# Performance work log

Hardware: AMD Instinct MI355X
Metric: run time of the kernel (lower is better)

Reference implementation:

```python
import jax, jax.numpy as jnp
import numpy as np

DIM = 256
HEADS = 8
HEAD_DIM = DIM // HEADS
B = 8
HH, WW = 32, 32
N = HH * WW
TABLE = (2 * HH - 1) * (2 * WW - 1)  # 3969
CPB_HID = 512


def _l2norm(t, eps=1e-12):
    # matches torch F.normalize(dim=-1): x / max(||x||, eps)
    n = jnp.sqrt(jnp.sum(t * t, axis=-1, keepdims=True))
    return t / jnp.maximum(n, eps)


def setup_inputs() -> dict:
    key = jax.random.key(0)
    ks = jax.random.split(key, 12)
    x = jax.random.normal(ks[0], (B, N, DIM), dtype=jnp.float32)
    relative_pos_index = jax.random.randint(ks[1], (N, N), 0, TABLE)
    relative_coords_table = jax.random.normal(ks[2], (TABLE, 2), dtype=jnp.float32)
    s = 0.02
    qkv_w = jax.random.normal(ks[3], (3 * DIM, DIM), dtype=jnp.float32) * s
    qkv_b = jnp.zeros((3 * DIM,), dtype=jnp.float32)
    query_embedding = jax.random.normal(ks[4], (HEADS, 1, HEAD_DIM), dtype=jnp.float32) * s
    # temperature init: log(exp(1/0.24) - 1) so softplus(temperature) = 1/0.24
    temperature = jnp.full((HEADS, 1, 1), float(np.log(np.expm1(1.0 / 0.24))), dtype=jnp.float32)
    proj_w = jax.random.normal(ks[5], (DIM, DIM), dtype=jnp.float32) * s
    proj_b = jnp.zeros((DIM,), dtype=jnp.float32)
    cpb_fc1_w = jax.random.normal(ks[6], (CPB_HID, 2), dtype=jnp.float32) * s
    cpb_fc1_b = jnp.zeros((CPB_HID,), dtype=jnp.float32)
    cpb_fc2_w = jax.random.normal(ks[7], (HEADS, CPB_HID), dtype=jnp.float32) * s
    cpb_fc2_b = jnp.zeros((HEADS,), dtype=jnp.float32)
    return dict(x=x, H=HH, W=WW, relative_pos_index=relative_pos_index,
                relative_coords_table=relative_coords_table,
                qkv_w=qkv_w, qkv_b=qkv_b, query_embedding=query_embedding,
                temperature=temperature, proj_w=proj_w, proj_b=proj_b,
                cpb_fc1_w=cpb_fc1_w, cpb_fc1_b=cpb_fc1_b,
                cpb_fc2_w=cpb_fc2_w, cpb_fc2_b=cpb_fc2_b)


def reference(x, H, W, relative_pos_index, relative_coords_table,
              qkv_w, qkv_b, query_embedding, temperature,
              proj_w, proj_b, cpb_fc1_w, cpb_fc1_b, cpb_fc2_w, cpb_fc2_b):
    Bc, Nc, C = x.shape
    seq_length_scale = jnp.asarray(np.log(HH * WW), dtype=x.dtype)  # from init input_resolution
    # qkv projection -> [B, heads, N, head_dim] each
    qkv = (x @ qkv_w.T + qkv_b).reshape(Bc, Nc, 3 * HEADS, HEAD_DIM).transpose(0, 2, 1, 3)
    q, k, v = qkv[:, :HEADS], qkv[:, HEADS:2 * HEADS], qkv[:, 2 * HEADS:]
    # CPB relative position bias: small MLP over coord table, then NxN gather
    h = jax.nn.relu(relative_coords_table @ cpb_fc1_w.T + cpb_fc1_b)  # [T, 512]
    table = (h @ cpb_fc2_w.T + cpb_fc2_b).T                           # [heads, T]
    rel_bias = table[:, relative_pos_index.reshape(-1)].reshape(HEADS, Nc, Nc)
    # cosine attention with learned temperature
    qn = _l2norm(q) + query_embedding[None]                           # [B, heads, N, hd]
    scale = jax.nn.softplus(temperature) * seq_length_scale           # [heads, 1, 1]
    attn = jnp.einsum('bhnd,bhmd->bhnm', qn * scale[None], _l2norm(k)) + rel_bias[None]
    attn = jax.nn.softmax(attn, axis=-1)
    out = jnp.einsum('bhnm,bhmd->bhnd', attn, v).transpose(0, 2, 1, 3).reshape(Bc, Nc, C)
    return out @ proj_w.T + proj_b
```

## Files before the change

kernel.cpp:

```cpp
#include <hip/hip_runtime.h>
#include <hip/hip_bf16.h>
#include <cstddef>
#include <cstdint>

typedef float v4f __attribute__((ext_vector_type(4)));
typedef short v8s __attribute__((ext_vector_type(8)));

__device__ __forceinline__ uint32_t fbits(float x){ uint32_t u; __builtin_memcpy(&u,&x,4); return u; }
__device__ __forceinline__ float ffrom(uint32_t u){ float f; __builtin_memcpy(&f,&u,4); return f; }
__device__ __forceinline__ short bf_rh(float x){ return (short)((fbits(x)+0x8000u)>>16); }
__device__ __forceinline__ uint32_t pack_bf_rh(float a, float b){
    uint32_t ua = fbits(a)+0x8000u, ub = fbits(b)+0x8000u;
#if __has_builtin(__builtin_amdgcn_perm)
    return __builtin_amdgcn_perm(ub, ua, 0x07060302u);
#else
    return (ua>>16) | (ub & 0xFFFF0000u);
#endif
}
#if __has_builtin(__builtin_amdgcn_exp2f)
#define EXP2(x) __builtin_amdgcn_exp2f(x)
#else
#define EXP2(x) exp2f(x)
#endif

__device__ __forceinline__ void gld16(const void* g, void* l) {
    __builtin_amdgcn_global_load_lds(
        (const __attribute__((address_space(1))) unsigned int*)g,
        (__attribute__((address_space(3))) unsigned int*)l, 16, 0, 0);
}
#define MFMA(a,b,c) __builtin_amdgcn_mfma_f32_16x16x32_bf16((a),(b),(c),0,0,0)

#define LOG2E 1.4426950408889634f

__global__ __launch_bounds__(256)
void cpb_kernel(const float* __restrict__ rct,
                const float* __restrict__ fc1w, const float* __restrict__ fc1b,
                const float* __restrict__ fc2w, const float* __restrict__ fc2b,
                float* __restrict__ table)
{
    __shared__ float s1[128];
    __shared__ float sb[64];
    __shared__ float s2[8][64];
    int tid = threadIdx.x;
    int jc  = blockIdx.y;
    int j0  = jc * 64;
    if (tid < 128) s1[tid] = fc1w[j0*2 + tid];
    else if (tid < 192) sb[tid-128] = fc1b[j0 + tid - 128];
    for (int i = tid; i < 512; i += 256) s2[i >> 6][i & 63] = fc2w[(i>>6)*512 + j0 + (i & 63)];
    __syncthreads();
    int r = blockIdx.x * 256 + tid;
    bool ok = r < 3969;
    float c0 = ok ? rct[2*r]   : 0.f;
    float c1 = ok ? rct[2*r+1] : 0.f;
    float a[8] = {0,0,0,0,0,0,0,0};
    #pragma unroll 4
    for (int j = 0; j < 64; ++j) {
        float hv = fmaxf(c0*s1[2*j] + c1*s1[2*j+1] + sb[j], 0.0f);
        #pragma unroll
        for (int hh = 0; hh < 8; ++hh) a[hh] += hv * s2[hh][j];
    }
    if (ok) {
        #pragma unroll
        for (int hh = 0; hh < 8; ++hh)
            atomicAdd(&table[hh*3969 + r], a[hh] + (jc == 0 ? fc2b[hh] : 0.f));
    }
}

__global__ __launch_bounds__(256)
void bias_mat(const float* __restrict__ tblf, const int* __restrict__ rpi,
              short* __restrict__ biasM)
{
    __shared__ float tb[3969];
    int h   = blockIdx.x >> 6;
    int q16 = blockIdx.x & 63;
    int tid = threadIdx.x;
    int w = tid >> 6, lane = tid & 63, t = lane & 15, quad = lane >> 4;
    for (int i = tid; i < 3969; i += 256) tb[i] = tblf[h*3969 + i] * LOG2E;
    __syncthreads();
    int row0 = q16*16 + quad*4;
    #pragma unroll 1
    for (int kk = 0; kk < 4; ++kk) {
        int kt = w*4 + kk;
        #pragma unroll
        for (int g = 0; g < 4; ++g) {
            float o[4];
            #pragma unroll
            for (int r = 0; r < 4; ++r)
                o[r] = tb[rpi[(size_t)(row0 + r)*1024 + kt*64 + 4*t + g]];
            uint2 pk;
            pk.x = pack_bf_rh(o[0], o[1]);
            pk.y = pack_bf_rh(o[2], o[3]);
            size_t base = ((((size_t)(h*64 + q16)*16 + kt)*4 + g)*64 + lane)*4;
            *(uint2*)(biasM + base) = pk;
        }
    }
}

__global__ __launch_bounds__(256)
void split_kernel(const float* __restrict__ x,  short* __restrict__ xh,  short* __restrict__ xl,
                  const float* __restrict__ wq, short* __restrict__ wqh, short* __restrict__ wql,
                  const float* __restrict__ wp, short* __restrict__ wph, short* __restrict__ wpl)
{
    int bid = blockIdx.x;
    const float* src; short* dh; short* dl; int base8;
    if (bid < 1024)      { src = x;  dh = xh;  dl = xl;  base8 = bid * 256; }
    else if (bid < 1120) { src = wq; dh = wqh; dl = wql; base8 = (bid-1024) * 256; }
    else                 { src = wp; dh = wph; dl = wpl; base8 = (bid-1120) * 256; }
    int e0 = (base8 + (int)threadIdx.x) * 8;
    int m  = e0 >> 8;
    int k  = e0 & 255;
    int kt = k >> 6, c = (k >> 3) & 7;
    float4 f0 = *(const float4*)(src + e0);
    float4 f1 = *(const float4*)(src + e0 + 4);
    float v[8] = {f0.x,f0.y,f0.z,f0.w,f1.x,f1.y,f1.z,f1.w};
    v8s hi, lo;
    #pragma unroll
    for (int j = 0; j < 8; ++j) {
        uint32_t u1 = fbits(v[j]) + 0x8000u;
        hi[j] = (short)(u1 >> 16);
        lo[j] = bf_rh(v[j] - ffrom(u1 & 0xFFFF0000u));
    }
    int dst = m*256 + kt*64 + ((c ^ (m & 7)) << 3);
    *(v8s*)&dh[dst] = hi;
    *(v8s*)&dl[dst] = lo;
}

template<int MODE, int PASSES>
__global__ __launch_bounds__(256)
void gemm_mfma(const short* __restrict__ Ahi, const short* __restrict__ Alo,
               const short* __restrict__ Whi, const short* __restrict__ Wlo,
               const float* __restrict__ bias, float* __restrict__ C,
               short* __restrict__ qhi, short* __restrict__ qlo,
               short* __restrict__ khi, short* __restrict__ klo,
               short* __restrict__ vt,
               const float* __restrict__ qe, const float* __restrict__ temp,
               int N)
{
    __shared__ __align__(16) char smem[49152];
    short* Ah = (short*)smem;
    short* Al = Ah + 128*64;
    short* Wh = Al + 128*64;
    short* Wl = Wh + 64*64;

    int tid  = threadIdx.x;
    int w    = tid >> 6;
    int lane = tid & 63;
    int t    = lane & 15;
    int quad = lane >> 4;
    int m0 = blockIdx.y * 128, n0 = blockIdx.x * 64;
    int Mw = (w >> 1) * 64, Nw = (w & 1) * 32;
    const bool onep = (PASSES == 1) || (MODE == 1 && n0 >= 512);

    v4f acc[4][2];
    #pragma unroll
    for (int mt = 0; mt < 4; ++mt)
        #pragma unroll
        for (int nt = 0; nt < 2; ++nt) acc[mt][nt] = (v4f){0,0,0,0};

    int lr8 = lane >> 3, lc8 = lane & 7;
    #pragma unroll 1
    for (int kt = 0; kt < 4; ++kt) {
        __syncthreads();
        #pragma unroll
        for (int i = 0; i < 4; ++i) {
            size_t grow = (size_t)(m0 + w*32 + i*8 + lr8) * 256 + kt*64 + lc8*8;
            int ls = (w*32 + i*8) * 64;
            gld16(Ahi + grow, Ah + ls);
            if (!onep) gld16(Alo + grow, Al + ls);
        }
        #pragma unroll
        for (int i = 0; i < 2; ++i) {
            size_t grow = (size_t)(n0 + w*16 + i*8 + lr8) * 256 + kt*64 + lc8*8;
            int ls = (w*16 + i*8) * 64;
            gld16(Whi + grow, Wh + ls);
            if (!onep) gld16(Wlo + grow, Wl + ls);
        }
        __syncthreads();
        #pragma unroll
        for (int kk = 0; kk < 2; ++kk) {
            int cp = ((kk*4 + quad) ^ (t & 7)) << 3;
            v8s bh8[2], bl8[2];
            #pragma unroll
            for (int nt = 0; nt < 2; ++nt) {
                int rowi = Nw + nt*16 + t;
                bh8[nt] = *(const v8s*)&Wh[rowi*64 + cp];
                if (!onep) bl8[nt] = *(const v8s*)&Wl[rowi*64 + cp];
            }
            #pragma unroll
            for (int mt = 0; mt < 4; ++mt) {
                int rowi = Mw + mt*16 + t;
                v8s ah = *(const v8s*)&Ah[rowi*64 + cp];
                v8s al;
                if (!onep) al = *(const v8s*)&Al[rowi*64 + cp];
                #pragma unroll
                for (int nt = 0; nt < 2; ++nt) {
                    acc[mt][nt] = MFMA(ah, bh8[nt], acc[mt][nt]);
                    if (!onep) {
                        acc[mt][nt] = MFMA(al, bh8[nt], acc[mt][nt]);
                        acc[mt][nt] = MFMA(ah, bl8[nt], acc[mt][nt]);
                    }
                }
            }
        }
    }

    #pragma unroll
    for (int nt = 0; nt < 2; ++nt) {
        float bv = bias[n0 + Nw + nt*16 + t];
        #pragma unroll
        for (int mt = 0; mt < 4; ++mt)
            #pragma unroll
            for (int r = 0; r < 4; ++r) acc[mt][nt][r] += bv;
    }

    if (MODE == 0) {
        #pragma unroll
        for (int mt = 0; mt < 4; ++mt)
            #pragma unroll
            for (int r = 0; r < 4; ++r) {
                int m = m0 + Mw + mt*16 + quad*4 + r;
                #pragma unroll
                for (int nt = 0; nt < 2; ++nt) {
                    int n = n0 + Nw + nt*16 + t;
                    C[(size_t)m * N + n] = acc[mt][nt][r];
                }
            }
    } else {
        int which = n0 >> 8;
        if (which < 2) {
            int head = ((n0 + Nw) >> 5) & 7;
            float scale = 0.f;
            if (which == 0)
                scale = log1pf(__expf(temp[head])) * 10.0f;
            #pragma unroll
            for (int mt = 0; mt < 4; ++mt)
                #pragma unroll
                for (int r = 0; r < 4; ++r) {
                    float a0 = acc[mt][0][r], a1 = acc[mt][1][r];
                    float s = a0*a0 + a1*a1;
                    s += __shfl_xor(s, 1); s += __shfl_xor(s, 2);
                    s += __shfl_xor(s, 4); s += __shfl_xor(s, 8);
                    float inv = 1.0f / fmaxf(sqrtf(s), 1e-12f);
                    int m = m0 + Mw + mt*16 + quad*4 + r;
                    int b = m >> 10, nrow = m & 1023;
                    if (which == 0) {
                        size_t rowoff = (((size_t)b*8 + head)*1024 + nrow) * 32;
                        #pragma unroll
                        for (int nt = 0; nt < 2; ++nt) {
                            int d = nt*16 + t;
                            float val = (acc[mt][nt][r] * inv + qe[head*32 + d]) * scale;
                            uint32_t u1 = fbits(val) + 0x8000u;
                            qhi[rowoff + d] = (short)(u1 >> 16);
                            qlo[rowoff + d] = bf_rh(val - ffrom(u1 & 0xFFFF0000u));
                        }
                    } else {
                        int kk = nrow & 63;
                        int p  = (kk & 3)*16 + (kk >> 2);
                        int prow = (nrow & ~63) | p;
                        int swk = (kk >> 3) & 3;
                        size_t rowoff = (((size_t)b*8 + head)*1024 + prow) * 32;
                        #pragma unroll
                        for (int nt = 0; nt < 2; ++nt) {
                            int d = nt*16 + t;
                            int c = d >> 3;
                            int dpos = ((c ^ swk) << 3) | (d & 7);
                            float val = acc[mt][nt][r] * inv;
                            uint32_t u1 = fbits(val) + 0x8000u;
                            khi[rowoff + dpos] = (short)(u1 >> 16);
                            klo[rowoff + dpos] = bf_rh(val - ffrom(u1 & 0xFFFF0000u));
                        }
                    }
                }
        } else {
            __syncthreads();
            short* VT = (short*)smem;
            #pragma unroll
            for (int mt = 0; mt < 4; ++mt)
                #pragma unroll
                for (int nt = 0; nt < 2; ++nt) {
                    int cl = Nw + nt*16 + t;
                    #pragma unroll
                    for (int r = 0; r < 4; ++r) {
                        int rl = Mw + mt*16 + quad*4 + r;
                        VT[cl*136 + rl] = bf_rh(acc[mt][nt][r]);
                    }
                }
            __syncthreads();
            int b = m0 >> 10;
            int keybase = m0 & 1023;
            int headbase = ((n0 - 512) >> 5) & 7;
            int cl = tid >> 2;
            int dim = cl & 31;
            int hd  = headbase + (cl >> 5);
            size_t obase = (((size_t)b*8 + hd)*32 + dim) * 1024 + keybase;
            #pragma unroll
            for (int p = 0; p < 4; ++p) {
                int ci  = (tid & 3) * 4 + p;
                int ktl = ci >> 3, c = ci & 7;
                v8s val = *(const v8s*)&VT[cl*136 + ktl*64 + c*8];
                *(v8s*)&vt[obase + ktl*64 + ((c ^ (dim & 7)) << 3)] = val;
            }
        }
    }
}

__global__ __launch_bounds__(256)
void attn_mfma(const short* __restrict__ qhi, const short* __restrict__ qlo,
               const short* __restrict__ khi, const short* __restrict__ klo,
               const short* __restrict__ vt,  const short* __restrict__ biasM,
               short* __restrict__ yhi)
{
    __shared__ __align__(16) short Khi_s[2][2048];
    __shared__ __align__(16) short Klo_s[2][2048];
    __shared__ __align__(16) short Vt_s[2][2048];
    __shared__ __align__(16) short Ps[4][16][68];

    int bh  = blockIdx.x >> 4;
    int qt  = blockIdx.x & 15;
    int h   = bh & 7;
    int b   = bh >> 3;
    int tid = threadIdx.x;
    int w    = tid >> 6;
    int lane = tid & 63;
    int t    = lane & 15;
    int quad = lane >> 4;

    size_t qoff = ((size_t)bh*1024 + qt*64 + w*16 + t) * 32 + quad*8;
    v8s qfh = *(const v8s*)(qhi + qoff);
    v8s qfl = *(const v8s*)(qlo + qoff);

    v4f Oacc[2] = {{0,0,0,0},{0,0,0,0}};
    float lsum[4] = {0,0,0,0};

    size_t kgbase = (size_t)bh * 32768;
    const short* bmb = biasM + ((size_t)(h*64 + qt*4 + w) * 16) * 1024 + lane*4;
    int qrow0 = qt*64 + w*16 + quad*4;
    int swzS = (quad ^ ((t >> 1) & 3)) << 3;
    int lr8 = lane >> 3, lc8 = lane & 7;

    gld16(khi + kgbase + w*512 + lane*8, &Khi_s[0][w*512]);
    gld16(klo + kgbase + w*512 + lane*8, &Klo_s[0][w*512]);
    gld16(vt + kgbase + (size_t)(w*8 + lr8)*1024 + lc8*8, &Vt_s[0][w*512]);
    uint2 curb[4];
    #pragma unroll
    for (int g = 0; g < 4; ++g) curb[g] = *(const uint2*)(bmb + g*256);

    #pragma unroll 1
    for (int kt = 0; kt < 16; ++kt) {
        int cur = kt & 1;
        __syncthreads();
        uint2 nxtb[4];
        if (kt < 15) {
            int nkt = kt + 1, nb = cur ^ 1;
            gld16(khi + kgbase + (size_t)nkt*2048 + w*512 + lane*8, &Khi_s[nb][w*512]);
            gld16(klo + kgbase + (size_t)nkt*2048 + w*512 + lane*8, &Klo_s[nb][w*512]);
            gld16(vt + kgbase + (size_t)(w*8 + lr8)*1024 + nkt*64 + lc8*8, &Vt_s[nb][w*512]);
            const short* bp = bmb + (size_t)nkt*1024;
            #pragma unroll
            for (int g = 0; g < 4; ++g) nxtb[g] = *(const uint2*)(bp + g*256);
        }

        v4f S[4];
        #pragma unroll
        for (int g = 0; g < 4; ++g) {
            v8s bh8 = *(const v8s*)&Khi_s[cur][(g*16 + t)*32 + swzS];
            v8s bl8 = *(const v8s*)&Klo_s[cur][(g*16 + t)*32 + swzS];
            v4f c;
            c[0] = ffrom(curb[g].x << 16);
            c[1] = ffrom(curb[g].x & 0xFFFF0000u);
            c[2] = ffrom(curb[g].y << 16);
            c[3] = ffrom(curb[g].y & 0xFFFF0000u);
            c = MFMA(qfh, bh8, c);
            c = MFMA(qfl, bh8, c);
            c = MFMA(qfh, bl8, c);
            S[g] = c;
        }

        #pragma unroll
        for (int r = 0; r < 4; ++r) {
            float p0 = EXP2(S[0][r]);
            float p1 = EXP2(S[1][r]);
            float p2 = EXP2(S[2][r]);
            float p3 = EXP2(S[3][r]);
            lsum[r] += (p0 + p1) + (p2 + p3);
            uint2 pk;
            pk.x = pack_bf_rh(p0, p1);
            pk.y = pack_bf_rh(p2, p3);
            *(uint2*)&Ps[w][quad*4 + r][t*4] = pk;
        }

        #pragma unroll
        for (int ks = 0; ks < 2; ++ks) {
            v8s pf = *(const v8s*)&Ps[w][t][ks*32 + quad*8];
            int vsw = ((ks*4 + quad) ^ (t & 7)) << 3;
            #pragma unroll
            for (int g = 0; g < 2; ++g) {
                v8s vf = *(const v8s*)&Vt_s[cur][(g*16 + t)*64 + vsw];
                Oacc[g] = MFMA(pf, vf, Oacc[g]);
            }
        }
        #pragma unroll
        for (int g = 0; g < 4; ++g) curb[g] = nxtb[g];
    }

    #pragma unroll
    for (int r = 0; r < 4; ++r) {
        float l = lsum[r];
        l += __shfl_xor(l, 1); l += __shfl_xor(l, 2);
        l += __shfl_xor(l, 4); l += __shfl_xor(l, 8);
        float inv = 1.0f / l;
        int qrow = qrow0 + r;
        int m = b*1024 + qrow;
        size_t mbase = (size_t)m * 256;
        int mk = m & 7;
        #pragma unroll
        for (int g = 0; g < 2; ++g) {
            float o = Oacc[g][r] * inv;
            int c = h*4 + g*2 + (t >> 3);
            int chp = ((c ^ mk) << 3) | (t & 7);
            yhi[mbase + chp] = bf_rh(o);
        }
    }
}

extern "C" void kernel_launch(void* const* d_in, const int* in_sizes, int n_in,
                              void* d_out, int out_size, void* d_ws, size_t ws_size,
                              hipStream_t stream)
{
    const float* x     = (const float*)d_in[0];
    const int*   rpi   = (const int*)d_in[3];
    const float* rct   = (const float*)d_in[4];
    const float* qkvw  = (const float*)d_in[5];
    const float* qkvb  = (const float*)d_in[6];
    const float* qe    = (const float*)d_in[7];
    const float* temp  = (const float*)d_in[8];
    const float* projw = (const float*)d_in[9];
    const float* projb = (const float*)d_in[10];
    const float* fc1w  = (const float*)d_in[11];
    const float* fc1b  = (const float*)d_in[12];
    const float* fc2w  = (const float*)d_in[13];
    const float* fc2b  = (const float*)d_in[14];

    char* p = (char*)d_ws;
    float* tblf  = (float*)p;  p += 131072;
    short* xh    = (short*)p;  p += 4194304;
    short* xl    = (short*)p;  p += 4194304;
    short* wqh   = (short*)p;  p += 393216;
    short* wql   = (short*)p;  p += 393216;
    short* wph   = (short*)p;  p += 131072;
    short* wpl   = (short*)p;  p += 131072;
    short* qh    = (short*)p;  p += 4194304;
    short* ql    = (short*)p;  p += 4194304;
    short* kh    = (short*)p;  p += 4194304;
    short* kl    = (short*)p;  p += 4194304;
    short* vt    = (short*)p;  p += 4194304;
    short* biasM = (short*)p;  p += 16777216;
    float* out   = (float*)d_out;

    hipMemsetAsync(tblf, 0, 8*3969*sizeof(float), stream);
    cpb_kernel<<<dim3(16,8), 256, 0, stream>>>(rct, fc1w, fc1b, fc2w, fc2b, tblf);

    bias_mat<<<512, 256, 0, stream>>>(tblf, rpi, biasM);

    split_kernel<<<1152, 256, 0, stream>>>(x, xh, xl, qkvw, wqh, wql, projw, wph, wpl);

    dim3 g1(768/64, 8192/128);
    gemm_mfma<1,3><<<g1, 256, 0, stream>>>(xh, xl, wqh, wql, qkvb, nullptr,
                                           qh, ql, kh, kl, vt, qe, temp, 768);

    attn_mfma<<<1024, 256, 0, stream>>>(qh, ql, kh, kl, vt, biasM, xh);

    dim3 g2(256/64, 8192/128);
    gemm_mfma<0,1><<<g2, 256, 0, stream>>>(xh, nullptr, wph, nullptr, projb, out,
                                           nullptr, nullptr, nullptr, nullptr,
                                           nullptr, nullptr, nullptr, 256);
}
```

Baseline: 169.2 us.

## Replace split-bf16 three-pass MFMA with single-pass fp16 MFMA across pipeline

Drops the hi/lo bf16 splitting of activations, weights, Q and K. Each is now a single fp16 value, and both the QKV GEMM and the attention QK^T use one fp16 MFMA instead of three bf16 MFMAs. This removes the lo buffers, their global traffic and LDS staging, and two thirds of the MFMA work in those stages. The CPB bias kernel is also restructured: each block loads the full MLP weights and reduces partial sums with shuffles, replacing atomics and a memset. The trade-off is lower mantissa precision than the split scheme and reliance on fp16 range.

```diff
diff --git a/kernel.cpp b/kernel.cpp
--- a/kernel.cpp
+++ b/kernel.cpp
@@ -5,6 +5,7 @@
 
 typedef float v4f __attribute__((ext_vector_type(4)));
 typedef short v8s __attribute__((ext_vector_type(8)));
+typedef _Float16 v8h __attribute__((ext_vector_type(8)));
 
 __device__ __forceinline__ uint32_t fbits(float x){ uint32_t u; __builtin_memcpy(&u,&x,4); return u; }
 __device__ __forceinline__ float ffrom(uint32_t u){ float f; __builtin_memcpy(&f,&u,4); return f; }
@@ -17,6 +18,8 @@
     return (ua>>16) | (ub & 0xFFFF0000u);
 #endif
 }
+__device__ __forceinline__ short f2h(float x){ _Float16 h = (_Float16)x; short s; __builtin_memcpy(&s,&h,2); return s; }
+__device__ __forceinline__ v8h as_h(v8s s){ v8h h; __builtin_memcpy(&h,&s,16); return h; }
 #if __has_builtin(__builtin_amdgcn_exp2f)
 #define EXP2(x) __builtin_amdgcn_exp2f(x)
 #else
@@ -28,7 +31,8 @@
         (const __attribute__((address_space(1))) unsigned int*)g,
         (__attribute__((address_space(3))) unsigned int*)l, 16, 0, 0);
 }
-#define MFMA(a,b,c) __builtin_amdgcn_mfma_f32_16x16x32_bf16((a),(b),(c),0,0,0)
+#define MFMA(a,b,c)  __builtin_amdgcn_mfma_f32_16x16x32_bf16((a),(b),(c),0,0,0)
+#define MFMAH(a,b,c) __builtin_amdgcn_mfma_f32_16x16x32_f16((a),(b),(c),0,0,0)
 
 #define LOG2E 1.4426950408889634f
 
@@ -38,31 +42,35 @@
                 const float* __restrict__ fc2w, const float* __restrict__ fc2b,
                 float* __restrict__ table)
 {
-    __shared__ float s1[128];
-    __shared__ float sb[64];
-    __shared__ float s2[8][64];
+    __shared__ float s1[1024];
+    __shared__ float sb[512];
+    __shared__ float s2[4096];
     int tid = threadIdx.x;
-    int jc  = blockIdx.y;
-    int j0  = jc * 64;
-    if (tid < 128) s1[tid] = fc1w[j0*2 + tid];
-    else if (tid < 192) sb[tid-128] = fc1b[j0 + tid - 128];
-    for (int i = tid; i < 512; i += 256) s2[i >> 6][i & 63] = fc2w[(i>>6)*512 + j0 + (i & 63)];
+    for (int i = tid; i < 1024; i += 256) s1[i] = fc1w[i];
+    for (int i = tid; i < 512;  i += 256) sb[i] = fc1b[i];
+    for (int i = tid; i < 4096; i += 256) s2[i] = fc2w[i];
     __syncthreads();
-    int r = blockIdx.x * 256 + tid;
-    bool ok = r < 3969;
+    int rl = tid >> 2, jp = tid & 3;
+    bool ok = rl < 63;
+    int r = blockIdx.x * 63 + rl;
     float c0 = ok ? rct[2*r]   : 0.f;
     float c1 = ok ? rct[2*r+1] : 0.f;
     float a[8] = {0,0,0,0,0,0,0,0};
+    int j0 = jp * 128;
     #pragma unroll 4
-    for (int j = 0; j < 64; ++j) {
+    for (int j = j0; j < j0 + 128; ++j) {
         float hv = fmaxf(c0*s1[2*j] + c1*s1[2*j+1] + sb[j], 0.0f);
         #pragma unroll
-        for (int hh = 0; hh < 8; ++hh) a[hh] += hv * s2[hh][j];
-    }
-    if (ok) {
-        #pragma unroll
-        for (int hh = 0; hh < 8; ++hh)
-            atomicAdd(&table[hh*3969 + r], a[hh] + (jc == 0 ? fc2b[hh] : 0.f));
+        for (int hh = 0; hh < 8; ++hh) a[hh] += hv * s2[hh*512 + j];
+    }
+    #pragma unroll
+    for (int hh = 0; hh < 8; ++hh) {
+        a[hh] += __shfl_xor(a[hh], 1);
+        a[hh] += __shfl_xor(a[hh], 2);
+    }
+    if (ok && jp == 0) {
+        #pragma unroll
+        for (int hh = 0; hh < 8; ++hh) table[hh*3969 + r] = a[hh] + fc2b[hh];
     }
 }
 
@@ -97,15 +105,15 @@
 }
 
 __global__ __launch_bounds__(256)
-void split_kernel(const float* __restrict__ x,  short* __restrict__ xh,  short* __restrict__ xl,
-                  const float* __restrict__ wq, short* __restrict__ wqh, short* __restrict__ wql,
-                  const float* __restrict__ wp, short* __restrict__ wph, short* __restrict__ wpl)
+void split_kernel(const float* __restrict__ x,  short* __restrict__ xh,
+                  const float* __restrict__ wq, short* __restrict__ wqh,
+                  const float* __restrict__ wp, short* __restrict__ wph)
 {
     int bid = blockIdx.x;
-    const float* src; short* dh; short* dl; int base8;
-    if (bid < 1024)      { src = x;  dh = xh;  dl = xl;  base8 = bid * 256; }
-    else if (bid < 1120) { src = wq; dh = wqh; dl = wql; base8 = (bid-1024) * 256; }
-    else                 { src = wp; dh = wph; dl = wpl; base8 = (bid-1120) * 256; }
+    const float* src; short* dh; int base8;
+    if (bid < 1024)      { src = x;  dh = xh;  base8 = bid * 256; }
+    else if (bid < 1120) { src = wq; dh = wqh; base8 = (bid-1024) * 256; }
+    else                 { src = wp; dh = wph; base8 = (bid-1120) * 256; }
     int e0 = (base8 + (int)threadIdx.x) * 8;
     int m  = e0 >> 8;
     int k  = e0 & 255;
@@ -113,34 +121,25 @@
     float4 f0 = *(const float4*)(src + e0);
     float4 f1 = *(const float4*)(src + e0 + 4);
     float v[8] = {f0.x,f0.y,f0.z,f0.w,f1.x,f1.y,f1.z,f1.w};
-    v8s hi, lo;
-    #pragma unroll
-    for (int j = 0; j < 8; ++j) {
-        uint32_t u1 = fbits(v[j]) + 0x8000u;
-        hi[j] = (short)(u1 >> 16);
-        lo[j] = bf_rh(v[j] - ffrom(u1 & 0xFFFF0000u));
-    }
+    v8s hi;
+    #pragma unroll
+    for (int j = 0; j < 8; ++j) hi[j] = f2h(v[j]);
     int dst = m*256 + kt*64 + ((c ^ (m & 7)) << 3);
     *(v8s*)&dh[dst] = hi;
-    *(v8s*)&dl[dst] = lo;
-}
-
-template<int MODE, int PASSES>
+}
+
+template<int MODE>
 __global__ __launch_bounds__(256)
-void gemm_mfma(const short* __restrict__ Ahi, const short* __restrict__ Alo,
-               const short* __restrict__ Whi, const short* __restrict__ Wlo,
+void gemm_mfma(const short* __restrict__ Ah_g, const short* __restrict__ Wh_g,
                const float* __restrict__ bias, float* __restrict__ C,
-               short* __restrict__ qhi, short* __restrict__ qlo,
-               short* __restrict__ khi, short* __restrict__ klo,
+               short* __restrict__ qh, short* __restrict__ kh,
                short* __restrict__ vt,
                const float* __restrict__ qe, const float* __restrict__ temp,
                int N)
 {
-    __shared__ __align__(16) char smem[49152];
+    __shared__ __align__(16) char smem[24576];
     short* Ah = (short*)smem;
-    short* Al = Ah + 128*64;
-    short* Wh = Al + 128*64;
-    short* Wl = Wh + 64*64;
+    short* Wh = Ah + 128*64;
 
     int tid  = threadIdx.x;
     int w    = tid >> 6;
@@ -149,7 +148,6 @@
     int quad = lane >> 4;
     int m0 = blockIdx.y * 128, n0 = blockIdx.x * 64;
     int Mw = (w >> 1) * 64, Nw = (w & 1) * 32;
-    const bool onep = (PASSES == 1) || (MODE == 1 && n0 >= 512);
 
     v4f acc[4][2];
     #pragma unroll
@@ -164,42 +162,27 @@
         #pragma unroll
         for (int i = 0; i < 4; ++i) {
             size_t grow = (size_t)(m0 + w*32 + i*8 + lr8) * 256 + kt*64 + lc8*8;
-            int ls = (w*32 + i*8) * 64;
-            gld16(Ahi + grow, Ah + ls);
-            if (!onep) gld16(Alo + grow, Al + ls);
+            gld16(Ah_g + grow, Ah + (w*32 + i*8) * 64);
         }
         #pragma unroll
         for (int i = 0; i < 2; ++i) {
             size_t grow = (size_t)(n0 + w*16 + i*8 + lr8) * 256 + kt*64 + lc8*8;
-            int ls = (w*16 + i*8) * 64;
-            gld16(Whi + grow, Wh + ls);
-            if (!onep) gld16(Wlo + grow, Wl + ls);
+            gld16(Wh_g + grow, Wh + (w*16 + i*8) * 64);
         }
         __syncthreads();
         #pragma unroll
         for (int kk = 0; kk < 2; ++kk) {
             int cp = ((kk*4 + quad) ^ (t & 7)) << 3;
-            v8s bh8[2], bl8[2];
-            #pragma unroll
-            for (int nt = 0; nt < 2; ++nt) {
-                int rowi = Nw + nt*16 + t;
-                bh8[nt] = *(const v8s*)&Wh[rowi*64 + cp];
-                if (!onep) bl8[nt] = *(const v8s*)&Wl[rowi*64 + cp];
-            }
+            v8h bh8[2];
+            #pragma unroll
+            for (int nt = 0; nt < 2; ++nt)
+                bh8[nt] = *(const v8h*)&Wh[(Nw + nt*16 + t)*64 + cp];
             #pragma unroll
             for (int mt = 0; mt < 4; ++mt) {
-                int rowi = Mw + mt*16 + t;
-                v8s ah = *(const v8s*)&Ah[rowi*64 + cp];
-                v8s al;
-                if (!onep) al = *(const v8s*)&Al[rowi*64 + cp];
+                v8h ah = *(const v8h*)&Ah[(Mw + mt*16 + t)*64 + cp];
                 #pragma unroll
-                for (int nt = 0; nt < 2; ++nt) {
-                    acc[mt][nt] = MFMA(ah, bh8[nt], acc[mt][nt]);
-                    if (!onep) {
-                        acc[mt][nt] = MFMA(al, bh8[nt], acc[mt][nt]);
-                        acc[mt][nt] = MFMA(ah, bl8[nt], acc[mt][nt]);
-                    }
-                }
+                for (int nt = 0; nt < 2; ++nt)
+                    acc[mt][nt] = MFMAH(ah, bh8[nt], acc[mt][nt]);
             }
         }
     }
@@ -220,10 +203,8 @@
             for (int r = 0; r < 4; ++r) {
                 int m = m0 + Mw + mt*16 + quad*4 + r;
                 #pragma unroll
-                for (int nt = 0; nt < 2; ++nt) {
-                    int n = n0 + Nw + nt*16 + t;
-                    C[(size_t)m * N + n] = acc[mt][nt][r];
-                }
+                for (int nt = 0; nt < 2; ++nt)
+                    C[(size_t)m * N + n0 + Nw + nt*16 + t] = acc[mt][nt][r];
             }
     } else {
         int which = n0 >> 8;
@@ -249,9 +230,7 @@
                         for (int nt = 0; nt < 2; ++nt) {
                             int d = nt*16 + t;
                             float val = (acc[mt][nt][r] * inv + qe[head*32 + d]) * scale;
-                            uint32_t u1 = fbits(val) + 0x8000u;
-                            qhi[rowoff + d] = (short)(u1 >> 16);
-                            qlo[rowoff + d] = bf_rh(val - ffrom(u1 & 0xFFFF0000u));
+                            qh[rowoff + d] = f2h(val);
                         }
                     } else {
                         int kk = nrow & 63;
@@ -262,12 +241,8 @@
                         #pragma unroll
                         for (int nt = 0; nt < 2; ++nt) {
                             int d = nt*16 + t;
-                            int c = d >> 3;
-                            int dpos = ((c ^ swk) << 3) | (d & 7);
-                            float val = acc[mt][nt][r] * inv;
-                            uint32_t u1 = fbits(val) + 0x8000u;
-                            khi[rowoff + dpos] = (short)(u1 >> 16);
-                            klo[rowoff + dpos] = bf_rh(val - ffrom(u1 & 0xFFFF0000u));
+                            int dpos = (((d >> 3) ^ swk) << 3) | (d & 7);
+                            kh[rowoff + dpos] = f2h(acc[mt][nt][r] * inv);
                         }
                     }
                 }
@@ -305,13 +280,11 @@
 }
 
 __global__ __launch_bounds__(256)
-void attn_mfma(const short* __restrict__ qhi, const short* __restrict__ qlo,
-               const short* __restrict__ khi, const short* __restrict__ klo,
+void attn_mfma(const short* __restrict__ qh, const short* __restrict__ kh,
                const short* __restrict__ vt,  const short* __restrict__ biasM,
-               short* __restrict__ yhi)
-{
-    __shared__ __align__(16) short Khi_s[2][2048];
-    __shared__ __align__(16) short Klo_s[2][2048];
+               short* __restrict__ yh)
+{
+    __shared__ __align__(16) short Kh_s[2][2048];
     __shared__ __align__(16) short Vt_s[2][2048];
     __shared__ __align__(16) short Ps[4][16][68];
 
@@ -326,8 +299,7 @@
     int quad = lane >> 4;
 
     size_t qoff = ((size_t)bh*1024 + qt*64 + w*16 + t) * 32 + quad*8;
-    v8s qfh = *(const v8s*)(qhi + qoff);
-    v8s qfl = *(const v8s*)(qlo + qoff);
+    v8h qf = *(const v8h*)(qh + qoff);
 
     v4f Oacc[2] = {{0,0,0,0},{0,0,0,0}};
     float lsum[4] = {0,0,0,0};
@@ -338,8 +310,7 @@
     int swzS = (quad ^ ((t >> 1) & 3)) << 3;
     int lr8 = lane >> 3, lc8 = lane & 7;
 
-    gld16(khi + kgbase + w*512 + lane*8, &Khi_s[0][w*512]);
-    gld16(klo + kgbase + w*512 + lane*8, &Klo_s[0][w*512]);
+    gld16(kh + kgbase + w*512 + lane*8, &Kh_s[0][w*512]);
     gld16(vt + kgbase + (size_t)(w*8 + lr8)*1024 + lc8*8, &Vt_s[0][w*512]);
     uint2 curb[4];
     #pragma unroll
@@ -352,8 +323,7 @@
         uint2 nxtb[4];
         if (kt < 15) {
             int nkt = kt + 1, nb = cur ^ 1;
-            gld16(khi + kgbase + (size_t)nkt*2048 + w*512 + lane*8, &Khi_s[nb][w*512]);
-            gld16(klo + kgbase + (size_t)nkt*2048 + w*512 + lane*8, &Klo_s[nb][w*512]);
+            gld16(kh + kgbase + (size_t)nkt*2048 + w*512 + lane*8, &Kh_s[nb][w*512]);
             gld16(vt + kgbase + (size_t)(w*8 + lr8)*1024 + nkt*64 + lc8*8, &Vt_s[nb][w*512]);
             const short* bp = bmb + (size_t)nkt*1024;
             #pragma unroll
@@ -363,17 +333,13 @@
         v4f S[4];
         #pragma unroll
         for (int g = 0; g < 4; ++g) {
-            v8s bh8 = *(const v8s*)&Khi_s[cur][(g*16 + t)*32 + swzS];
-            v8s bl8 = *(const v8s*)&Klo_s[cur][(g*16 + t)*32 + swzS];
+            v8h kb = *(const v8h*)&Kh_s[cur][(g*16 + t)*32 + swzS];
             v4f c;
             c[0] = ffrom(curb[g].x << 16);
             c[1] = ffrom(curb[g].x & 0xFFFF0000u);
             c[2] = ffrom(curb[g].y << 16);
             c[3] = ffrom(curb[g].y & 0xFFFF0000u);
-            c = MFMA(qfh, bh8, c);
-            c = MFMA(qfl, bh8, c);
-            c = MFMA(qfh, bl8, c);
-            S[g] = c;
+            S[g] = MFMAH(qf, kb, c);
         }
 
         #pragma unroll
@@ -418,7 +384,7 @@
             float o = Oacc[g][r] * inv;
             int c = h*4 + g*2 + (t >> 3);
             int chp = ((c ^ mk) << 3) | (t & 7);
-            yhi[mbase + chp] = bf_rh(o);
+            yh[mbase + chp] = f2h(o);
         }
     }
 }
@@ -444,34 +410,28 @@
     char* p = (char*)d_ws;
     float* tblf  = (float*)p;  p += 131072;
     short* xh    = (short*)p;  p += 4194304;
-    short* xl    = (short*)p;  p += 4194304;
     short* wqh   = (short*)p;  p += 393216;
-    short* wql   = (short*)p;  p += 393216;
     short* wph   = (short*)p;  p += 131072;
-    short* wpl   = (short*)p;  p += 131072;
     short* qh    = (short*)p;  p += 4194304;
-    short* ql    = (short*)p;  p += 4194304;
     short* kh    = (short*)p;  p += 4194304;
-    short* kl    = (short*)p;  p += 4194304;
     short* vt    = (short*)p;  p += 4194304;
     short* biasM = (short*)p;  p += 16777216;
     float* out   = (float*)d_out;
 
-    hipMemsetAsync(tblf, 0, 8*3969*sizeof(float), stream);
-    cpb_kernel<<<dim3(16,8), 256, 0, stream>>>(rct, fc1w, fc1b, fc2w, fc2b, tblf);
+    cpb_kernel<<<63, 256, 0, stream>>>(rct, fc1w, fc1b, fc2w, fc2b, tblf);
 
     bias_mat<<<512, 256, 0, stream>>>(tblf, rpi, biasM);
 
-    split_kernel<<<1152, 256, 0, stream>>>(x, xh, xl, qkvw, wqh, wql, projw, wph, wpl);
+    split_kernel<<<1152, 256, 0, stream>>>(x, xh, qkvw, wqh, projw, wph);
 
     dim3 g1(768/64, 8192/128);
-    gemm_mfma<1,3><<<g1, 256, 0, stream>>>(xh, xl, wqh, wql, qkvb, nullptr,
-                                           qh, ql, kh, kl, vt, qe, temp, 768);
-
-    attn_mfma<<<1024, 256, 0, stream>>>(qh, ql, kh, kl, vt, biasM, xh);
+    gemm_mfma<1><<<g1, 256, 0, stream>>>(xh, wqh, qkvb, nullptr,
+                                         qh, kh, vt, qe, temp, 768);
+
+    attn_mfma<<<1024, 256, 0, stream>>>(qh, kh, vt, biasM, xh);
 
     dim3 g2(256/64, 8192/128);
-    gemm_mfma<0,1><<<g2, 256, 0, stream>>>(xh, nullptr, wph, nullptr, projb, out,
-                                           nullptr, nullptr, nullptr, nullptr,
-                                           nullptr, nullptr, nullptr, 256);
-}
+    gemm_mfma<0><<<g2, 256, 0, stream>>>(xh, wph, projb, out,
+                                         nullptr, nullptr, nullptr,
+                                         nullptr, nullptr, 256);
+}
```

Result: faster. 159.8 us (-5.6%).
